# Performance work log

Hardware: AMD Instinct MI355X
Metric: run time of the kernel (lower is better)

Reference implementation:

```python
import jax
import jax.numpy as jnp
from jax import lax
import numpy as np

INPUT_DIM = 784
HIDDEN_DIM = 1024
BATCH = 256
N_BINS = 10


def setup_inputs() -> dict:
    key = jax.random.key(0)
    k1, k2, k3, k4, k5 = jax.random.split(key, 5)
    # kaiming-normal-ish init scales (faithful in spirit; exact values irrelevant for math)
    W = jax.random.normal(k1, (HIDDEN_DIM, INPUT_DIM), dtype=jnp.float32) * np.sqrt(2.0 / INPUT_DIM)
    c = jnp.zeros((HIDDEN_DIM, 1), dtype=jnp.float32)
    V = jax.random.normal(k2, (INPUT_DIM, HIDDEN_DIM, N_BINS), dtype=jnp.float32) * np.sqrt(2.0 / N_BINS)
    b = jnp.zeros((INPUT_DIM, N_BINS), dtype=jnp.float32)
    x = jax.random.randint(k3, (BATCH, INPUT_DIM), 0, N_BINS, dtype=jnp.int32)
    return {"x": x, "W": W, "c": c, "V": V, "b": b}


def reference(x, W, c, V, b):
    # x: [B, D] int pixel bins; W: [H, D]; c: [H, 1]; V: [D, H, 10]; b: [D, 10]
    B = x.shape[0]
    xf = x.astype(jnp.float32)  # [B, D]
    a0 = jnp.broadcast_to(c[:, 0][None, :], (B, W.shape[0]))  # [B, H]

    def step(a, inp):
        Vi, bi, Wi, xi = inp  # Vi:[H,10], bi:[10], Wi:[H], xi:[B]
        h = jax.nn.sigmoid(a)                       # [B, H]
        p = jax.nn.softmax(h @ Vi + bi, axis=1)     # [B, 10]
        a = a + xi[:, None] * Wi[None, :]           # rank-1 update, matches x_i @ W[:,i].T
        return a, p

    _, p_seq = lax.scan(step, a0, (V, b, W.T, xf.T))  # p_seq: [D, B, 10]
    p_hat = jnp.transpose(p_seq, (1, 2, 0))            # [B, 10, D] == torch.stack(p_hat, dim=2)
    return p_hat
```

## Files before the change

kernel.cpp:

```cpp
#include <hip/hip_runtime.h>
#include <stdint.h>

#define D_DIM 784
#define H_DIM 1024
#define B_DIM 256
#define NBIN  10
#define G_CH  8
#define T_CH  98
#define BT    16
#define BF    2
#define LOG2E 1.4426950408889634f

typedef _Float16 half8_t  __attribute__((ext_vector_type(8)));
typedef __fp16   fp16x2_t __attribute__((ext_vector_type(2)));
typedef float    float4_t __attribute__((ext_vector_type(4)));

__global__ void k_prep(const float* __restrict__ W, const float* __restrict__ V,
                       _Float16* __restrict__ Wt2h, _Float16* __restrict__ VB) {
    __shared__ __align__(16) float smem[H_DIM * NBIN];
    int tid = threadIdx.x;
    if (blockIdx.x < D_DIM) {
        int i = blockIdx.x;
        const float4* src = (const float4*)(V + (size_t)i * H_DIM * NBIN);
        #pragma unroll
        for (int q = 0; q < 10; ++q) {
            float4 v = src[q * 256 + tid];
            *((float4*)&smem[(q * 256 + tid) * 4]) = v;
        }
        __syncthreads();
        #pragma unroll
        for (int q = 0; q < 8; ++q) {
            int pair = q * 256 + tid;
            int kk = pair >> 6, l = pair & 63;
            int n = l & 15, hb = kk * 32 + ((l >> 4) & 3) * 8;
            union { _Float16 h[8]; uint4 u; } o;
            #pragma unroll
            for (int jj = 0; jj < 8; ++jj)
                o.h[jj] = (_Float16)((n < NBIN) ? smem[(hb + jj) * NBIN + n] : 0.0f);
            ((uint4*)VB)[(size_t)i * 2048 + pair] = o.u;
        }
    } else {
        int q = blockIdx.x - D_DIM;
        int j0 = (q % 13) * 64, h0 = (q / 13) * 64;
        float (*t)[65] = (float(*)[65])smem;
        int tj = tid & 63, tr = tid >> 6;
        int j = j0 + tj;
        #pragma unroll
        for (int r = 0; r < 16; ++r) {
            int hh = tr * 16 + r;
            t[hh][tj] = (j < D_DIM) ? W[(size_t)(h0 + hh) * D_DIM + j] : 0.0f;
        }
        __syncthreads();
        #pragma unroll
        for (int r = 0; r < 16; ++r) {
            int jj = tr * 16 + r;
            int jo = j0 + jj;
            if (jo < D_DIM) Wt2h[(size_t)jo * H_DIM + h0 + tj] = (_Float16)(t[tj][jj] * LOG2E);
        }
    }
}

__global__ void k_pscan(const _Float16* __restrict__ Wt2h, const int* __restrict__ x,
                        const float* __restrict__ c, _Float16* __restrict__ PA) {
    int b0 = blockIdx.x * BF;
    int h  = blockIdx.y * 256 + threadIdx.x;
    __shared__ float xs[BF][D_DIM];
    for (int q = threadIdx.x; q < BF * (D_DIM / 4); q += 256) {
        int bb = q / (D_DIM / 4), r = q % (D_DIM / 4);
        int4 xi = ((const int4*)(x + (size_t)(b0 + bb) * D_DIM))[r];
        float4 xf = make_float4((float)xi.x, (float)xi.y, (float)xi.z, (float)xi.w);
        *((float4*)&xs[bb][r * 4]) = xf;
    }
    float acc0 = c[h] * LOG2E, acc1 = acc0;
    __syncthreads();
    for (int t = 0; t < T_CH; ++t) {
        PA[((size_t)t * B_DIM + b0 + 0) * H_DIM + h] = (_Float16)acc0;
        PA[((size_t)t * B_DIM + b0 + 1) * H_DIM + h] = (_Float16)acc1;
        #pragma unroll
        for (int j = 0; j < G_CH; ++j) {
            float wv = (float)Wt2h[(size_t)(t * G_CH + j) * H_DIM + h];
            acc0 += xs[0][t * G_CH + j] * wv;
            acc1 += xs[1][t * G_CH + j] * wv;
        }
    }
}

__global__ __launch_bounds__(256, 2)
void k_main(const _Float16* __restrict__ VB, const _Float16* __restrict__ Wt2h,
            const _Float16* __restrict__ PA, const int* __restrict__ x,
            const float* __restrict__ bias, float* __restrict__ out) {
    int bt  = blockIdx.x;
    int tc  = blockIdx.y;
    int tid = threadIdx.x;
    int w   = tid >> 6;
    int l   = tid & 63;
    int bl  = l & 15;
    int kg  = l >> 4;
    int bg  = bt * BT + bl;
    int i0  = tc * G_CH;

    __shared__ __align__(16) _Float16 wlds[G_CH][H_DIM];
    __shared__ float red[4][64][18];
    __shared__ float bs[G_CH][16];

    {
        int ii = tid >> 4, n = tid & 15;
        if (ii < G_CH) bs[ii][n] = (n < NBIN) ? bias[(size_t)(i0 + ii) * NBIN + n] : 0.0f;
    }
    {
        #pragma unroll
        for (int r = 0; r < G_CH; ++r) {
            uint2 v = ((const uint2*)(Wt2h + (size_t)(i0 + r) * H_DIM))[tid];
            *((uint2*)&wlds[r][tid * 4]) = v;
        }
    }
    float xvf[G_CH];
    {
        const int4* xp = (const int4*)(x + (size_t)bg * D_DIM + i0);
        int4 x0 = xp[0], x1 = xp[1];
        xvf[0] = (float)x0.x; xvf[1] = (float)x0.y; xvf[2] = (float)x0.z; xvf[3] = (float)x0.w;
        xvf[4] = (float)x1.x; xvf[5] = (float)x1.y; xvf[6] = (float)x1.z; xvf[7] = (float)x1.w;
    }
    float a[8][8];
    {
        const _Float16* src = PA + ((size_t)tc * B_DIM + bg) * H_DIM + w * 256 + kg * 8;
        #pragma unroll
        for (int m = 0; m < 8; ++m) {
            half8_t av = *((const half8_t*)(src + m * 32));
            #pragma unroll
            for (int j = 0; j < 8; ++j) a[m][j] = (float)av[j];
        }
    }
    __syncthreads();

    const uint4* vbbase = (const uint4*)VB + ((size_t)w * 8) * 64 + l;
    float4_t cf[G_CH];
    uint4 vb[8];

    {
        const uint4* p = vbbase + (size_t)i0 * 2048;
        #pragma unroll
        for (int m = 0; m < 8; ++m) vb[m] = p[m * 64];
    }

    auto compute_ii = [&](int ii) {
        int inext = i0 + ii + ((ii < G_CH - 1) ? 1 : 0);
        const uint4* pn = vbbase + (size_t)inext * 2048;
        float xf = xvf[ii];
        float4_t cfr = {0.f, 0.f, 0.f, 0.f};
        #pragma unroll
        for (int m = 0; m < 8; ++m) {
            union { half8_t h8; uint u32[4]; } af;
            #pragma unroll
            for (int p = 0; p < 4; ++p) {
                float s0 = __builtin_amdgcn_rcpf(1.0f + __builtin_amdgcn_exp2f(-a[m][2 * p]));
                float s1 = __builtin_amdgcn_rcpf(1.0f + __builtin_amdgcn_exp2f(-a[m][2 * p + 1]));
                union { fp16x2_t v; uint u; } cv;
                cv.v = __builtin_amdgcn_cvt_pkrtz(s0, s1);
                af.u32[p] = cv.u;
            }
            half8_t bv = __builtin_bit_cast(half8_t, vb[m]);
            cfr = __builtin_amdgcn_mfma_f32_16x16x32_f16(af.h8, bv, cfr, 0, 0, 0);
            vb[m] = pn[m * 64];
            half8_t wh = *((const half8_t*)&wlds[ii][w * 256 + kg * 8 + m * 32]);
            a[m][0] += xf * (float)wh[0]; a[m][1] += xf * (float)wh[1];
            a[m][2] += xf * (float)wh[2]; a[m][3] += xf * (float)wh[3];
            a[m][4] += xf * (float)wh[4]; a[m][5] += xf * (float)wh[5];
            a[m][6] += xf * (float)wh[6]; a[m][7] += xf * (float)wh[7];
        }
        cf[ii] = cfr;
    };

    auto softmax_store = [&](int half) {
        float p4[4];
        #pragma unroll
        for (int q = 0; q < 4; ++q) {
            int ii = half * 4 + q;
            float tot = red[0][l][q * 4 + w] + red[1][l][q * 4 + w]
                      + red[2][l][q * 4 + w] + red[3][l][q * 4 + w];
            float v = (bl < NBIN) ? tot + bs[ii][bl] : -3.0e38f;
            float vm = v;
            vm = fmaxf(vm, __shfl_xor(vm, 1));
            vm = fmaxf(vm, __shfl_xor(vm, 2));
            vm = fmaxf(vm, __shfl_xor(vm, 4));
            vm = fmaxf(vm, __shfl_xor(vm, 8));
            float e = __builtin_amdgcn_exp2f((v - vm) * LOG2E);
            float ss = e;
            ss += __shfl_xor(ss, 1); ss += __shfl_xor(ss, 2);
            ss += __shfl_xor(ss, 4); ss += __shfl_xor(ss, 8);
            p4[q] = e * __builtin_amdgcn_rcpf(ss);
        }
        if (bl < NBIN) {
            int b = bt * BT + kg * 4 + w;
            size_t base = ((size_t)b * NBIN + bl) * D_DIM + i0 + half * 4;
            float4 v = make_float4(p4[0], p4[1], p4[2], p4[3]);
            *((float4*)(out + base)) = v;
        }
    };

    compute_ii(0); compute_ii(1); compute_ii(2); compute_ii(3);
    #pragma unroll
    for (int q = 0; q < 4; ++q) {
        #pragma unroll
        for (int r = 0; r < 4; ++r) red[w][l][q * 4 + r] = cf[q][r];
    }
    __syncthreads();
    compute_ii(4); compute_ii(5); compute_ii(6); compute_ii(7);
    softmax_store(0);
    __syncthreads();
    #pragma unroll
    for (int q = 0; q < 4; ++q) {
        #pragma unroll
        for (int r = 0; r < 4; ++r) red[w][l][q * 4 + r] = cf[4 + q][r];
    }
    __syncthreads();
    softmax_store(1);
}

extern "C" void kernel_launch(void* const* d_in, const int* in_sizes, int n_in,
                              void* d_out, int out_size, void* d_ws, size_t ws_size,
                              hipStream_t stream) {
    const int*   x    = (const int*)d_in[0];
    const float* W    = (const float*)d_in[1];
    const float* c    = (const float*)d_in[2];
    const float* V    = (const float*)d_in[3];
    const float* bias = (const float*)d_in[4];
    float* out = (float*)d_out;

    char* ws = (char*)d_ws;
    size_t off = 0;
    _Float16* Wt2h = (_Float16*)(ws + off);
    off += (size_t)D_DIM * H_DIM * sizeof(_Float16);
    off = (off + 255) & ~(size_t)255;
    _Float16* VB = (_Float16*)(ws + off);
    off += (size_t)D_DIM * 32 * 64 * 8 * sizeof(_Float16);
    off = (off + 255) & ~(size_t)255;
    _Float16* PA = (_Float16*)(ws + off);

    k_prep<<<dim3(D_DIM + 208), 256, 0, stream>>>(W, V, Wt2h, VB);
    k_pscan<<<dim3(B_DIM / BF, 4), 256, 0, stream>>>(Wt2h, x, c, PA);
    k_main<<<dim3(B_DIM / BT, T_CH), 256, 0, stream>>>(VB, Wt2h, PA, x, bias, out);
}
```

Baseline: 188.5 us.

## Fold prefix-scan into prep kernel reading W directly, pad reduction LDS

The separate prefix-sum kernel is merged into the prep kernel as an extra 512 blocks that compute the chunked pre-activations from the original fp32 W rows, not from the transposed fp16 copy. This removes one launch and the dependency on the transpose finishing first, so the scan can run concurrently with the V and W repacking. The trade-off is that each thread now reads a strided W row (stride 784 floats across threads, so uncoalesced) and accumulates in full fp32 weights. The reduction LDS array in the main kernel is also padded from 18 to 19 to reduce bank conflicts.

```diff
diff --git a/kernel.cpp b/kernel.cpp
--- a/kernel.cpp
+++ b/kernel.cpp
@@ -16,7 +16,9 @@
 typedef float    float4_t __attribute__((ext_vector_type(4)));
 
 __global__ void k_prep(const float* __restrict__ W, const float* __restrict__ V,
-                       _Float16* __restrict__ Wt2h, _Float16* __restrict__ VB) {
+                       const int* __restrict__ x, const float* __restrict__ c,
+                       _Float16* __restrict__ Wt2h, _Float16* __restrict__ VB,
+                       _Float16* __restrict__ PA) {
     __shared__ __align__(16) float smem[H_DIM * NBIN];
     int tid = threadIdx.x;
     if (blockIdx.x < D_DIM) {
@@ -39,7 +41,7 @@
                 o.h[jj] = (_Float16)((n < NBIN) ? smem[(hb + jj) * NBIN + n] : 0.0f);
             ((uint4*)VB)[(size_t)i * 2048 + pair] = o.u;
         }
-    } else {
+    } else if (blockIdx.x < D_DIM + 208) {
         int q = blockIdx.x - D_DIM;
         int j0 = (q % 13) * 64, h0 = (q / 13) * 64;
         float (*t)[65] = (float(*)[65])smem;
@@ -57,30 +59,32 @@
             int jo = j0 + jj;
             if (jo < D_DIM) Wt2h[(size_t)jo * H_DIM + h0 + tj] = (_Float16)(t[tj][jj] * LOG2E);
         }
-    }
-}
-
-__global__ void k_pscan(const _Float16* __restrict__ Wt2h, const int* __restrict__ x,
-                        const float* __restrict__ c, _Float16* __restrict__ PA) {
-    int b0 = blockIdx.x * BF;
-    int h  = blockIdx.y * 256 + threadIdx.x;
-    __shared__ float xs[BF][D_DIM];
-    for (int q = threadIdx.x; q < BF * (D_DIM / 4); q += 256) {
-        int bb = q / (D_DIM / 4), r = q % (D_DIM / 4);
-        int4 xi = ((const int4*)(x + (size_t)(b0 + bb) * D_DIM))[r];
-        float4 xf = make_float4((float)xi.x, (float)xi.y, (float)xi.z, (float)xi.w);
-        *((float4*)&xs[bb][r * 4]) = xf;
-    }
-    float acc0 = c[h] * LOG2E, acc1 = acc0;
-    __syncthreads();
-    for (int t = 0; t < T_CH; ++t) {
-        PA[((size_t)t * B_DIM + b0 + 0) * H_DIM + h] = (_Float16)acc0;
-        PA[((size_t)t * B_DIM + b0 + 1) * H_DIM + h] = (_Float16)acc1;
-        #pragma unroll
-        for (int j = 0; j < G_CH; ++j) {
-            float wv = (float)Wt2h[(size_t)(t * G_CH + j) * H_DIM + h];
-            acc0 += xs[0][t * G_CH + j] * wv;
-            acc1 += xs[1][t * G_CH + j] * wv;
+    } else {
+        int p    = blockIdx.x - (D_DIM + 208);
+        int bblk = p & 127, hblk = p >> 7;
+        int b0   = bblk * BF;
+        int h    = hblk * 256 + tid;
+        float (*xs)[D_DIM] = (float(*)[D_DIM])smem;
+        for (int q = tid; q < BF * (D_DIM / 4); q += 256) {
+            int bb = q / (D_DIM / 4), r = q % (D_DIM / 4);
+            int4 xi = ((const int4*)(x + (size_t)(b0 + bb) * D_DIM))[r];
+            float4 xf = make_float4((float)xi.x * LOG2E, (float)xi.y * LOG2E,
+                                    (float)xi.z * LOG2E, (float)xi.w * LOG2E);
+            *((float4*)&xs[bb][r * 4]) = xf;
+        }
+        float acc0 = c[h] * LOG2E, acc1 = acc0;
+        __syncthreads();
+        const float4* wr = (const float4*)(W + (size_t)h * D_DIM);
+        for (int t = 0; t < T_CH; ++t) {
+            PA[((size_t)t * B_DIM + b0 + 0) * H_DIM + h] = (_Float16)acc0;
+            PA[((size_t)t * B_DIM + b0 + 1) * H_DIM + h] = (_Float16)acc1;
+            float4 wa = wr[t * 2], wb = wr[t * 2 + 1];
+            float wv[8] = {wa.x, wa.y, wa.z, wa.w, wb.x, wb.y, wb.z, wb.w};
+            #pragma unroll
+            for (int j = 0; j < 8; ++j) {
+                acc0 += xs[0][t * 8 + j] * wv[j];
+                acc1 += xs[1][t * 8 + j] * wv[j];
+            }
         }
     }
 }
@@ -100,7 +104,7 @@
     int i0  = tc * G_CH;
 
     __shared__ __align__(16) _Float16 wlds[G_CH][H_DIM];
-    __shared__ float red[4][64][18];
+    __shared__ float red[4][64][19];
     __shared__ float bs[G_CH][16];
 
     {
@@ -237,7 +241,6 @@
     off = (off + 255) & ~(size_t)255;
     _Float16* PA = (_Float16*)(ws + off);
 
-    k_prep<<<dim3(D_DIM + 208), 256, 0, stream>>>(W, V, Wt2h, VB);
-    k_pscan<<<dim3(B_DIM / BF, 4), 256, 0, stream>>>(Wt2h, x, c, PA);
+    k_prep<<<dim3(D_DIM + 208 + 512), 256, 0, stream>>>(W, V, x, c, Wt2h, VB, PA);
     k_main<<<dim3(B_DIM / BT, T_CH), 256, 0, stream>>>(VB, Wt2h, PA, x, bias, out);
 }
```

Result: slower. 199.1 us (+5.6%).
